# Kernel optimization log

Hardware: AMD Instinct MI355X
Metric: run time of the kernel (lower is better)

Reference implementation:

```python
import jax, jax.numpy as jnp
import numpy as np

N_NODES = 100000
N_EDGES = 1600000
N_GRAPHS = 1024
HID = 128
FINAL = 128
SPATIAL = 3
NUM_LAYERS = 3
VOCAB = 100


def _linear_params(key, d_in, d_out):
    k1, k2 = jax.random.split(key)
    s = 1.0 / np.sqrt(d_in)
    W = jax.random.uniform(k1, (d_out, d_in), jnp.float32, -s, s)
    b = jax.random.uniform(k2, (d_out,), jnp.float32, -s, s)
    return W, b


def setup_inputs() -> dict:
    key = jax.random.key(0)
    ks = jax.random.split(key, 16)
    z = jax.random.randint(ks[0], (N_NODES,), 0, VOCAB)
    pos = jax.random.normal(ks[1], (N_NODES, SPATIAL), jnp.float32)
    edge_index = jax.random.randint(ks[2], (2, N_EDGES), 0, N_NODES)
    batch = jnp.sort(jax.random.randint(ks[3], (N_NODES,), 0, N_GRAPHS))
    emb_table = jax.random.normal(ks[4], (VOCAB, HID), jnp.float32)
    W_pos, b_pos = _linear_params(ks[5], SPATIAL, HID)
    W_comb, b_comb = _linear_params(ks[6], 2 * HID, HID)
    # GIN: each conv's MLP is Linear(d,d) -> ReLU -> Linear(d,d); all dims 128 here.
    gW1, gb1, gW2, gb2 = [], [], [], []
    for i in range(NUM_LAYERS):
        k = jax.random.fold_in(ks[7], i)
        ka, kb = jax.random.split(k)
        W1, b1 = _linear_params(ka, HID, HID)
        W2, b2 = _linear_params(kb, HID, FINAL if i == NUM_LAYERS - 1 else HID)
        gW1.append(W1); gb1.append(b1); gW2.append(W2); gb2.append(b2)
    gin_W1 = jnp.stack(gW1); gin_b1 = jnp.stack(gb1)
    gin_W2 = jnp.stack(gW2); gin_b2 = jnp.stack(gb2)
    W_p1, b_p1 = _linear_params(ks[8], FINAL, FINAL)
    W_p2, b_p2 = _linear_params(ks[9], FINAL, 1)
    return {
        "z": z, "pos": pos, "edge_index": edge_index, "batch": batch,
        "emb_table": emb_table, "W_pos": W_pos, "b_pos": b_pos,
        "W_comb": W_comb, "b_comb": b_comb,
        "gin_W1": gin_W1, "gin_b1": gin_b1, "gin_W2": gin_W2, "gin_b2": gin_b2,
        "W_p1": W_p1, "b_p1": b_p1, "W_p2": W_p2, "b_p2": b_p2,
    }


def reference(z, pos, edge_index, batch, emb_table, W_pos, b_pos, W_comb, b_comb,
              gin_W1, gin_b1, gin_W2, gin_b2, W_p1, b_p1, W_p2, b_p2):
    src, dst = edge_index[0], edge_index[1]
    # initial node embedding: embed(z) || linear(pos) -> linear -> relu
    atom = emb_table[z]                                   # [N, H]
    pe = pos @ W_pos.T + b_pos                            # [N, H]
    x = jax.nn.relu(jnp.concatenate([atom, pe], axis=-1) @ W_comb.T + b_comb)
    # GIN layers: x' = MLP((1+eps)*x + sum_{j->i} x_j), eps=0; act between convs only
    for i in range(NUM_LAYERS):
        aggr = jax.ops.segment_sum(x[src], dst, num_segments=N_NODES)  # [N, H]
        h = aggr + x
        h = jax.nn.relu(h @ gin_W1[i].T + gin_b1[i])
        x = h @ gin_W2[i].T + gin_b2[i]
        if i < NUM_LAYERS - 1:
            x = jax.nn.relu(x)
    # sum pooling per graph, then predict MLP
    g = jax.ops.segment_sum(x, batch, num_segments=N_GRAPHS)  # [G, F]
    h = jax.nn.relu(g @ W_p1.T + b_p1)
    return h @ W_p2.T + b_p2                              # [G, 1]
```

## Files before the change

kernel.cpp:

```cpp
#include <hip/hip_runtime.h>
#include <hip/hip_bf16.h>

#define HID 128
#define CAP 64
#define NBK 2048

typedef __attribute__((ext_vector_type(8))) short bfrag;
typedef __attribute__((ext_vector_type(4))) float f32x4;

static inline size_t align256(size_t x) { return (x + 255) & ~(size_t)255; }

__device__ __forceinline__ unsigned short f2bf(float f) {
  unsigned int x = __float_as_uint(f);
  unsigned int r = x + 0x7fffu + ((x >> 16) & 1u);
  return (unsigned short)(r >> 16);
}
__device__ __forceinline__ float bflo(unsigned int u) { return __uint_as_float(u << 16); }
__device__ __forceinline__ float bfhi(unsigned int u) { return __uint_as_float(u & 0xffff0000u); }


__global__ __launch_bounds__(256) void k_prep(const int* __restrict__ src,
                                              const int* __restrict__ dst,
                                              int* __restrict__ cnt,
                                              int* __restrict__ bsrc, int E, int N,
                                              const float* __restrict__ W_comb,
                                              const float* __restrict__ gW1,
                                              const float* __restrict__ gW2,
                                              unsigned short* __restrict__ Wcb,
                                              unsigned short* __restrict__ W1b,
                                              unsigned short* __restrict__ W2b,
                                              const int* __restrict__ batch,
                                              int* __restrict__ goff, int G) {
  const int bid = blockIdx.x;
  const int tid = threadIdx.x;
  if (bid < NBK) {
    const int slice = bid & 7;
    const int sidx = bid >> 3;
    const int s_lo = (int)(((long long)slice * N) >> 3);
    const int s_hi = (int)(((long long)(slice + 1) * N) >> 3);
    for (int e = sidx * 256 + tid; e < E; e += (NBK / 8) * 256) {
      int d = dst[e];
      if (d >= s_lo && d < s_hi) {
        int slot = atomicAdd(&cnt[d], 1);
        if (slot < CAP) bsrc[(size_t)d * CAP + slot] = src[e];
      }
    }
  } else if (bid < NBK + 192) {
    int i = (bid - NBK) * 256 + tid;
    if (i < 128 * 256) Wcb[i] = f2bf(W_comb[i]);
    if (i < 3 * 128 * 128) {
      W1b[i] = f2bf(gW1[i]);
      W2b[i] = f2bf(gW2[i]);
    }
  } else {
    int g = (bid - NBK - 192) * 256 + tid;
    if (g <= G) {
      int lo = 0, hi = N;
      while (lo < hi) {
        int mid = (lo + hi) >> 1;
        if (batch[mid] < g) lo = mid + 1; else hi = mid;
      }
      goff[g] = lo;
    }
  }
}


__global__ __launch_bounds__(256, 2) void k_init_mm(const int* __restrict__ z,
                                                    const float* __restrict__ pos,
                                                    const float* __restrict__ emb,
                                                    const float* __restrict__ W_pos,
                                                    const float* __restrict__ b_pos,
                                                    const unsigned short* __restrict__ Wcb,
                                                    const float* __restrict__ bias,
                                                    const unsigned short* __restrict__ W1n,
                                                    unsigned short* __restrict__ Y, int n) {
  __shared__ unsigned int sE[32 * 128];
  __shared__ unsigned int sB[32 * 64];
  const int t = threadIdx.x;
  const int w = t >> 6, l = t & 63, lr = l & 15, lk = l >> 4;

  bfrag wcf[2][8];
#pragma unroll
  for (int s = 0; s < 2; ++s)
#pragma unroll
    for (int ks = 0; ks < 8; ++ks)
      wcf[s][ks] = *(const bfrag*)(Wcb + (size_t)(32 * w + 16 * s + lr) * 256 + ks * 32 + lk * 8);
  bfrag w1f[2][4];
#pragma unroll
  for (int s = 0; s < 2; ++s)
#pragma unroll
    for (int ks = 0; ks < 4; ++ks)
      w1f[s][ks] = *(const bfrag*)(W1n + (size_t)(32 * w + 16 * s + lr) * HID + ks * 32 + lk * 8);
  const float bias0 = bias[32 * w + lr];
  const float bias1 = bias[32 * w + 16 + lr];

  const int m0 = blockIdx.x * 32;
  {
    const int r = t >> 3, i = t & 7;
    int node = m0 + r;
    if (node >= n) node = n - 1;
    const int zz = z[node];
    const float p0 = pos[node * 3 + 0], p1 = pos[node * 3 + 1], p2 = pos[node * 3 + 2];
    const int swz = (r & 7) << 2;
#pragma unroll
    for (int k = 0; k < 16; ++k) {
      const int j = i + k * 8;
      float v0, v1;
      if (j < 64) {
        const float2 ev = *(const float2*)&emb[(size_t)zz * 128 + 2 * j];
        v0 = ev.x; v1 = ev.y;
      } else {
        const int f0 = 2 * j - 128;
        v0 = b_pos[f0] + W_pos[f0 * 3] * p0 + W_pos[f0 * 3 + 1] * p1 + W_pos[f0 * 3 + 2] * p2;
        v1 = b_pos[f0 + 1] + W_pos[f0 * 3 + 3] * p0 + W_pos[f0 * 3 + 4] * p1 +
             W_pos[f0 * 3 + 5] * p2;
      }
      sE[r * 128 + (j ^ swz)] = (unsigned int)f2bf(v0) | ((unsigned int)f2bf(v1) << 16);
    }
  }
  __syncthreads();

  f32x4 acc00 = {0.f, 0.f, 0.f, 0.f}, acc01 = acc00, acc10 = acc00, acc11 = acc00;
#pragma unroll
  for (int mt = 0; mt < 2; ++mt) {
    const int row = 16 * mt + lr;
    const int swz = (row & 7) << 2;
#pragma unroll
    for (int ks = 0; ks < 8; ++ks) {
      const bfrag a = *(const bfrag*)&sE[row * 128 + ((ks * 16 + lk * 4) ^ swz)];
      if (mt == 0) {
        acc00 = __builtin_amdgcn_mfma_f32_16x16x32_bf16(a, wcf[0][ks], acc00, 0, 0, 0);
        acc01 = __builtin_amdgcn_mfma_f32_16x16x32_bf16(a, wcf[1][ks], acc01, 0, 0, 0);
      } else {
        acc10 = __builtin_amdgcn_mfma_f32_16x16x32_bf16(a, wcf[0][ks], acc10, 0, 0, 0);
        acc11 = __builtin_amdgcn_mfma_f32_16x16x32_bf16(a, wcf[1][ks], acc11, 0, 0, 0);
      }
    }
  }
  {
    unsigned short* sB16 = (unsigned short*)sB;
#pragma unroll
    for (int mt = 0; mt < 2; ++mt) {
#pragma unroll
      for (int s = 0; s < 2; ++s) {
        const f32x4 a = mt == 0 ? (s == 0 ? acc00 : acc01) : (s == 0 ? acc10 : acc11);
        const float bb = s == 0 ? bias0 : bias1;
        const int col = 32 * w + 16 * s + lr;
#pragma unroll
        for (int r = 0; r < 4; ++r) {
          const int rowL = 16 * mt + 4 * lk + r;
          const int cu = (col >> 1) ^ ((rowL & 7) << 2);
          sB16[rowL * 128 + cu * 2 + (col & 1)] = f2bf(fmaxf(a[r] + bb, 0.f));
        }
      }
    }
  }
  __syncthreads();

  f32x4 u00 = {0.f, 0.f, 0.f, 0.f}, u01 = u00, u10 = u00, u11 = u00;
#pragma unroll
  for (int mt = 0; mt < 2; ++mt) {
    const int row = 16 * mt + lr;
    const int swz = (row & 7) << 2;
#pragma unroll
    for (int ks = 0; ks < 4; ++ks) {
      const bfrag a = *(const bfrag*)&sB[row * 64 + ((ks * 16 + lk * 4) ^ swz)];
      if (mt == 0) {
        u00 = __builtin_amdgcn_mfma_f32_16x16x32_bf16(a, w1f[0][ks], u00, 0, 0, 0);
        u01 = __builtin_amdgcn_mfma_f32_16x16x32_bf16(a, w1f[1][ks], u01, 0, 0, 0);
      } else {
        u10 = __builtin_amdgcn_mfma_f32_16x16x32_bf16(a, w1f[0][ks], u10, 0, 0, 0);
        u11 = __builtin_amdgcn_mfma_f32_16x16x32_bf16(a, w1f[1][ks], u11, 0, 0, 0);
      }
    }
  }
#pragma unroll
  for (int mt = 0; mt < 2; ++mt) {
#pragma unroll
    for (int s = 0; s < 2; ++s) {
      const f32x4 a = mt == 0 ? (s == 0 ? u00 : u01) : (s == 0 ? u10 : u11);
      const int col = 32 * w + 16 * s + lr;
#pragma unroll
      for (int r = 0; r < 4; ++r) {
        const int row = m0 + 16 * mt + 4 * lk + r;
        if (row < n) Y[(size_t)row * HID + col] = f2bf(a[r]);
      }
    }
  }
}


template <int LAST>
__global__ __launch_bounds__(256, 3) void k_layer(const unsigned int* __restrict__ U,
                                                  const int* __restrict__ cnt,
                                                  const int* __restrict__ bsrc,
                                                  const float* __restrict__ b1,
                                                  const unsigned short* __restrict__ W2b,
                                                  const float* __restrict__ b2,
                                                  const unsigned short* __restrict__ W1n,
                                                  unsigned short* __restrict__ Y, int n) {
  __shared__ unsigned int sA[32 * 64];
  __shared__ unsigned int sB[32 * 64];
  const int t = threadIdx.x;
  const int w = t >> 6, l = t & 63, lr = l & 15, lk = l >> 4;
  const int lgrp = lk, lpos = lr;

  bfrag w2f[2][4];
#pragma unroll
  for (int s = 0; s < 2; ++s)
#pragma unroll
    for (int ks = 0; ks < 4; ++ks)
      w2f[s][ks] = *(const bfrag*)(W2b + (size_t)(32 * w + 16 * s + lr) * HID + ks * 32 + lk * 8);
  bfrag w1f[2][4];
  if (!LAST) {
#pragma unroll
    for (int s = 0; s < 2; ++s)
#pragma unroll
      for (int ks = 0; ks < 4; ++ks)
        w1f[s][ks] = *(const bfrag*)(W1n + (size_t)(32 * w + 16 * s + lr) * HID + ks * 32 + lk * 8);
  }
  const float b2a = b2[32 * w + lr];
  const float b2b = b2[32 * w + 16 + lr];
  const float4 bb0 = *(const float4*)&b1[8 * lpos];
  const float4 bb1 = *(const float4*)&b1[8 * lpos + 4];
  const float ms = (lgrp == 0) ? 1.f : 0.f;

  const int m0 = blockIdx.x * 32;

  int degs[8];
  int eidxs[8];
#pragma unroll
  for (int ri = 0; ri < 8; ++ri) {
    int node = m0 + 8 * w + ri;
    if (node >= n) node = n - 1;
    int d = cnt[node];
    degs[ri] = d > CAP ? CAP : d;
    eidxs[ri] = bsrc[(size_t)node * CAP + l];
  }
#pragma unroll
  for (int ri = 0; ri < 8; ++ri) {
    const int row = 8 * w + ri;
    int node = m0 + row;
    if (node >= n) node = n - 1;
    const int deg = degs[ri];
    const int eidx = eidxs[ri];
    const uint4 sv = *(const uint4*)(U + (size_t)node * 64 + 4 * lpos);
    float a0 = ms * bflo(sv.x), a1 = ms * bfhi(sv.x);
    float a2 = ms * bflo(sv.y), a3 = ms * bfhi(sv.y);
    float a4 = ms * bflo(sv.z), a5 = ms * bfhi(sv.z);
    float a6 = ms * bflo(sv.w), a7 = ms * bfhi(sv.w);
    int k = 0;
    for (; k + 7 < deg; k += 8) {
      const int e0 = __shfl(eidx, k + lgrp);
      const int e1 = __shfl(eidx, k + 4 + lgrp);
      const uint4 u0 = *(const uint4*)(U + (size_t)e0 * 64 + 4 * lpos);
      const uint4 u1 = *(const uint4*)(U + (size_t)e1 * 64 + 4 * lpos);
      a0 += bflo(u0.x); a1 += bfhi(u0.x); a2 += bflo(u0.y); a3 += bfhi(u0.y);
      a4 += bflo(u0.z); a5 += bfhi(u0.z); a6 += bflo(u0.w); a7 += bfhi(u0.w);
      a0 += bflo(u1.x); a1 += bfhi(u1.x); a2 += bflo(u1.y); a3 += bfhi(u1.y);
      a4 += bflo(u1.z); a5 += bfhi(u1.z); a6 += bflo(u1.w); a7 += bfhi(u1.w);
    }
    for (; k < deg; k += 4) {
      int idx = k + lgrp;
      const float m = idx < deg ? 1.f : 0.f;
      if (idx >= deg) idx = deg - 1;
      const int e0 = __shfl(eidx, idx);
      const uint4 u0 = *(const uint4*)(U + (size_t)e0 * 64 + 4 * lpos);
      a0 += m * bflo(u0.x); a1 += m * bfhi(u0.x); a2 += m * bflo(u0.y); a3 += m * bfhi(u0.y);
      a4 += m * bflo(u0.z); a5 += m * bfhi(u0.z); a6 += m * bflo(u0.w); a7 += m * bfhi(u0.w);
    }
    a0 += __shfl_xor(a0, 16); a0 += __shfl_xor(a0, 32);
    a1 += __shfl_xor(a1, 16); a1 += __shfl_xor(a1, 32);
    a2 += __shfl_xor(a2, 16); a2 += __shfl_xor(a2, 32);
    a3 += __shfl_xor(a3, 16); a3 += __shfl_xor(a3, 32);
    a4 += __shfl_xor(a4, 16); a4 += __shfl_xor(a4, 32);
    a5 += __shfl_xor(a5, 16); a5 += __shfl_xor(a5, 32);
    a6 += __shfl_xor(a6, 16); a6 += __shfl_xor(a6, 32);
    a7 += __shfl_xor(a7, 16); a7 += __shfl_xor(a7, 32);
    if (lgrp == 0) {
      const int swz = (row & 7) << 2;
      uint4 o;
      o.x = (unsigned int)f2bf(fmaxf(a0 + bb0.x, 0.f)) |
            ((unsigned int)f2bf(fmaxf(a1 + bb0.y, 0.f)) << 16);
      o.y = (unsigned int)f2bf(fmaxf(a2 + bb0.z, 0.f)) |
            ((unsigned int)f2bf(fmaxf(a3 + bb0.w, 0.f)) << 16);
      o.z = (unsigned int)f2bf(fmaxf(a4 + bb1.x, 0.f)) |
            ((unsigned int)f2bf(fmaxf(a5 + bb1.y, 0.f)) << 16);
      o.w = (unsigned int)f2bf(fmaxf(a6 + bb1.z, 0.f)) |
            ((unsigned int)f2bf(fmaxf(a7 + bb1.w, 0.f)) << 16);
      *(uint4*)&sA[row * 64 + ((4 * lpos) ^ swz)] = o;
    }
  }
  __syncthreads();

  f32x4 acc00 = {0.f, 0.f, 0.f, 0.f}, acc01 = acc00, acc10 = acc00, acc11 = acc00;
#pragma unroll
  for (int mt = 0; mt < 2; ++mt) {
    const int row = 16 * mt + lr;
    const int swz = (row & 7) << 2;
#pragma unroll
    for (int ks = 0; ks < 4; ++ks) {
      const bfrag a = *(const bfrag*)&sA[row * 64 + ((ks * 16 + lk * 4) ^ swz)];
      if (mt == 0) {
        acc00 = __builtin_amdgcn_mfma_f32_16x16x32_bf16(a, w2f[0][ks], acc00, 0, 0, 0);
        acc01 = __builtin_amdgcn_mfma_f32_16x16x32_bf16(a, w2f[1][ks], acc01, 0, 0, 0);
      } else {
        acc10 = __builtin_amdgcn_mfma_f32_16x16x32_bf16(a, w2f[0][ks], acc10, 0, 0, 0);
        acc11 = __builtin_amdgcn_mfma_f32_16x16x32_bf16(a, w2f[1][ks], acc11, 0, 0, 0);
      }
    }
  }
  if (LAST) {
#pragma unroll
    for (int mt = 0; mt < 2; ++mt) {
#pragma unroll
      for (int s = 0; s < 2; ++s) {
        const f32x4 a = mt == 0 ? (s == 0 ? acc00 : acc01) : (s == 0 ? acc10 : acc11);
        const float bb = s == 0 ? b2a : b2b;
        const int col = 32 * w + 16 * s + lr;
#pragma unroll
        for (int r = 0; r < 4; ++r) {
          const int row = m0 + 16 * mt + 4 * lk + r;
          if (row < n) Y[(size_t)row * HID + col] = f2bf(a[r] + bb);
        }
      }
    }
  } else {
    unsigned short* sB16 = (unsigned short*)sB;
#pragma unroll
    for (int mt = 0; mt < 2; ++mt) {
#pragma unroll
      for (int s = 0; s < 2; ++s) {
        const f32x4 a = mt == 0 ? (s == 0 ? acc00 : acc01) : (s == 0 ? acc10 : acc11);
        const float bb = s == 0 ? b2a : b2b;
        const int col = 32 * w + 16 * s + lr;
#pragma unroll
        for (int r = 0; r < 4; ++r) {
          const int rowL = 16 * mt + 4 * lk + r;
          const int cu = (col >> 1) ^ ((rowL & 7) << 2);
          sB16[rowL * 128 + cu * 2 + (col & 1)] = f2bf(fmaxf(a[r] + bb, 0.f));
        }
      }
    }
    __syncthreads();
    f32x4 u00 = {0.f, 0.f, 0.f, 0.f}, u01 = u00, u10 = u00, u11 = u00;
#pragma unroll
    for (int mt = 0; mt < 2; ++mt) {
      const int row = 16 * mt + lr;
      const int swz = (row & 7) << 2;
#pragma unroll
      for (int ks = 0; ks < 4; ++ks) {
        const bfrag a = *(const bfrag*)&sB[row * 64 + ((ks * 16 + lk * 4) ^ swz)];
        if (mt == 0) {
          u00 = __builtin_amdgcn_mfma_f32_16x16x32_bf16(a, w1f[0][ks], u00, 0, 0, 0);
          u01 = __builtin_amdgcn_mfma_f32_16x16x32_bf16(a, w1f[1][ks], u01, 0, 0, 0);
        } else {
          u10 = __builtin_amdgcn_mfma_f32_16x16x32_bf16(a, w1f[0][ks], u10, 0, 0, 0);
          u11 = __builtin_amdgcn_mfma_f32_16x16x32_bf16(a, w1f[1][ks], u11, 0, 0, 0);
        }
      }
    }
#pragma unroll
    for (int mt = 0; mt < 2; ++mt) {
#pragma unroll
      for (int s = 0; s < 2; ++s) {
        const f32x4 a = mt == 0 ? (s == 0 ? u00 : u01) : (s == 0 ? u10 : u11);
        const int col = 32 * w + 16 * s + lr;
#pragma unroll
        for (int r = 0; r < 4; ++r) {
          const int row = m0 + 16 * mt + 4 * lk + r;
          if (row < n) Y[(size_t)row * HID + col] = f2bf(a[r]);
        }
      }
    }
  }
}


__global__ __launch_bounds__(128) void k_pool(const unsigned short* __restrict__ X,
                                              const int* __restrict__ goff,
                                              const float* __restrict__ Wp1,
                                              const float* __restrict__ bp1,
                                              const float* __restrict__ Wp2,
                                              const float* __restrict__ bp2,
                                              float* __restrict__ out, int G) {
  __shared__ float sg[HID];
  __shared__ float sred[HID];
  int g = blockIdx.x;
  int f = threadIdx.x;
  int n0 = goff[g], n1 = goff[g + 1];
  float c0 = 0.f, c1 = 0.f, c2 = 0.f, c3 = 0.f;
  int nn = n0;
  for (; nn + 3 < n1; nn += 4) {
    c0 += __uint_as_float((unsigned int)X[(size_t)nn * HID + f] << 16);
    c1 += __uint_as_float((unsigned int)X[(size_t)(nn + 1) * HID + f] << 16);
    c2 += __uint_as_float((unsigned int)X[(size_t)(nn + 2) * HID + f] << 16);
    c3 += __uint_as_float((unsigned int)X[(size_t)(nn + 3) * HID + f] << 16);
  }
  for (; nn < n1; ++nn) c0 += __uint_as_float((unsigned int)X[(size_t)nn * HID + f] << 16);
  sg[f] = (c0 + c1) + (c2 + c3);
  __syncthreads();
  float a0 = 0.f, a1 = 0.f, a2 = 0.f, a3 = 0.f;
#pragma unroll
  for (int k4 = 0; k4 < 32; ++k4) {
    float4 wv = *(const float4*)&Wp1[f * HID + k4 * 4];
    float4 xv = *(const float4*)&sg[k4 * 4];
    a0 += wv.x * xv.x; a1 += wv.y * xv.y; a2 += wv.z * xv.z; a3 += wv.w * xv.w;
  }
  float h = fmaxf(bp1[f] + ((a0 + a1) + (a2 + a3)), 0.f);
  sred[f] = Wp2[f] * h;
  __syncthreads();
  for (int s = 64; s > 0; s >>= 1) {
    if (f < s) sred[f] += sred[f + s];
    __syncthreads();
  }
  if (f == 0) out[g] = sred[0] + bp2[0];
}


extern "C" void kernel_launch(void* const* d_in, const int* in_sizes, int n_in,
                              void* d_out, int out_size, void* d_ws, size_t ws_size,
                              hipStream_t stream) {
  const int*   z      = (const int*)d_in[0];
  const float* pos    = (const float*)d_in[1];
  const int*   ei     = (const int*)d_in[2];
  const int*   batch  = (const int*)d_in[3];
  const float* emb    = (const float*)d_in[4];
  const float* W_pos  = (const float*)d_in[5];
  const float* b_pos  = (const float*)d_in[6];
  const float* W_comb = (const float*)d_in[7];
  const float* b_comb = (const float*)d_in[8];
  const float* gW1    = (const float*)d_in[9];
  const float* gb1    = (const float*)d_in[10];
  const float* gW2    = (const float*)d_in[11];
  const float* gb2    = (const float*)d_in[12];
  const float* Wp1    = (const float*)d_in[13];
  const float* bp1    = (const float*)d_in[14];
  const float* Wp2    = (const float*)d_in[15];
  const float* bp2    = (const float*)d_in[16];
  float* out = (float*)d_out;

  const int N = in_sizes[0];
  const int E = in_sizes[2] / 2;
  const int G = out_size;
  const int* srcp = ei;
  const int* dstp = ei + E;
  const int ntiles = (N + 31) / 32;

  char* w = (char*)d_ws;
  unsigned short* Ub  = (unsigned short*)w; w += align256((size_t)N * 128 * 2);
  unsigned short* Vb  = (unsigned short*)w; w += align256((size_t)N * 128 * 2);
  unsigned short* Wcb = (unsigned short*)w; w += align256((size_t)128 * 256 * 2);
  unsigned short* W1b = (unsigned short*)w; w += align256((size_t)3 * 128 * 128 * 2);
  unsigned short* W2b = (unsigned short*)w; w += align256((size_t)3 * 128 * 128 * 2);
  int* cnt  = (int*)w; w += align256((size_t)N * 4);
  int* bsrc = (int*)w; w += align256((size_t)N * CAP * 4);
  int* goff = (int*)w; w += align256((size_t)(G + 1) * 4);

  hipMemsetAsync(cnt, 0, (size_t)N * 4, stream);

  k_prep<<<NBK + 192 + 5, 256, 0, stream>>>(srcp, dstp, cnt, bsrc, E, N,
                                            W_comb, gW1, gW2, Wcb, W1b, W2b,
                                            batch, goff, G);

  k_init_mm<<<ntiles, 256, 0, stream>>>(z, pos, emb, W_pos, b_pos, Wcb, b_comb,
                                        W1b, Ub, N);

  k_layer<0><<<ntiles, 256, 0, stream>>>((const unsigned int*)Ub, cnt, bsrc, gb1,
                                         W2b, gb2, W1b + (size_t)1 * 128 * 128, Vb, N);
  k_layer<0><<<ntiles, 256, 0, stream>>>((const unsigned int*)Vb, cnt, bsrc, gb1 + 128,
                                         W2b + (size_t)1 * 128 * 128, gb2 + 128,
                                         W1b + (size_t)2 * 128 * 128, Ub, N);
  k_layer<1><<<ntiles, 256, 0, stream>>>((const unsigned int*)Ub, cnt, bsrc, gb1 + 256,
                                         W2b + (size_t)2 * 128 * 128, gb2 + 256,
                                         (const unsigned short*)nullptr, Vb, N);

  k_pool<<<G, HID, 0, stream>>>(Vb, goff, Wp1, bp1, Wp2, bp2, out, G);
}
```

Before: 431.9 us.

## Merge prep and init kernels; pad gather with zero sentinel row

Fuses the CSR-bucket/weight-conversion prep kernel and the initial embedding matmul into one launch. The init blocks now convert W_comb and layer-0 W1 to bf16 straight from fp32 instead of waiting for a converted copy, which removes one launch and the dependency between them. The layer gather loop now rounds each degree up to a multiple of 8 and sends padded slots to an extra all-zero row N in U/V, so the masked tail loop goes away. The cost is some extra zero-row loads and the extra per-block conversion work in the init blocks.

```diff
diff --git a/kernel.cpp b/kernel.cpp
--- a/kernel.cpp
+++ b/kernel.cpp
@@ -4,6 +4,7 @@
 #define HID 128
 #define CAP 64
 #define NBK 2048
+#define NWC 192
 
 typedef __attribute__((ext_vector_type(8))) short bfrag;
 typedef __attribute__((ext_vector_type(4))) float f32x4;
@@ -18,21 +19,35 @@
 __device__ __forceinline__ float bflo(unsigned int u) { return __uint_as_float(u << 16); }
 __device__ __forceinline__ float bfhi(unsigned int u) { return __uint_as_float(u & 0xffff0000u); }
 
-
-__global__ __launch_bounds__(256) void k_prep(const int* __restrict__ src,
-                                              const int* __restrict__ dst,
-                                              int* __restrict__ cnt,
-                                              int* __restrict__ bsrc, int E, int N,
-                                              const float* __restrict__ W_comb,
-                                              const float* __restrict__ gW1,
-                                              const float* __restrict__ gW2,
-                                              unsigned short* __restrict__ Wcb,
-                                              unsigned short* __restrict__ W1b,
-                                              unsigned short* __restrict__ W2b,
-                                              const int* __restrict__ batch,
-                                              int* __restrict__ goff, int G) {
+__device__ __forceinline__ bfrag load8bf(const float* __restrict__ p) {
+  const float4 a = *(const float4*)p;
+  const float4 b = *(const float4*)(p + 4);
+  bfrag r;
+  r[0] = (short)f2bf(a.x); r[1] = (short)f2bf(a.y);
+  r[2] = (short)f2bf(a.z); r[3] = (short)f2bf(a.w);
+  r[4] = (short)f2bf(b.x); r[5] = (short)f2bf(b.y);
+  r[6] = (short)f2bf(b.z); r[7] = (short)f2bf(b.w);
+  return r;
+}
+
+
+__global__ __launch_bounds__(256, 2) void k_mega(
+    const int* __restrict__ src, const int* __restrict__ dst,
+    int* __restrict__ cnt, int* __restrict__ bsrc, int E, int N,
+    const float* __restrict__ gW1, const float* __restrict__ gW2,
+    unsigned short* __restrict__ W1b, unsigned short* __restrict__ W2b,
+    const int* __restrict__ batch, int* __restrict__ goff, int G, int initBase,
+    const int* __restrict__ z, const float* __restrict__ pos,
+    const float* __restrict__ emb, const float* __restrict__ W_pos,
+    const float* __restrict__ b_pos, const float* __restrict__ W_comb,
+    const float* __restrict__ b_comb,
+    unsigned int* __restrict__ UbZ, unsigned int* __restrict__ VbZ,
+    unsigned short* __restrict__ Y, int n) {
+  __shared__ unsigned int sE[32 * 128];
+  __shared__ unsigned int sB[32 * 64];
   const int bid = blockIdx.x;
   const int tid = threadIdx.x;
+
   if (bid < NBK) {
     const int slice = bid & 7;
     const int sidx = bid >> 3;
@@ -45,15 +60,18 @@
         if (slot < CAP) bsrc[(size_t)d * CAP + slot] = src[e];
       }
     }
-  } else if (bid < NBK + 192) {
+    return;
+  }
+  if (bid < NBK + NWC) {
     int i = (bid - NBK) * 256 + tid;
-    if (i < 128 * 256) Wcb[i] = f2bf(W_comb[i]);
     if (i < 3 * 128 * 128) {
       W1b[i] = f2bf(gW1[i]);
       W2b[i] = f2bf(gW2[i]);
     }
-  } else {
-    int g = (bid - NBK - 192) * 256 + tid;
+    return;
+  }
+  if (bid < initBase) {
+    int g = (bid - NBK - NWC) * 256 + tid;
     if (g <= G) {
       int lo = 0, hi = N;
       while (lo < hi) {
@@ -62,42 +80,33 @@
       }
       goff[g] = lo;
     }
-  }
-}
-
-
-__global__ __launch_bounds__(256, 2) void k_init_mm(const int* __restrict__ z,
-                                                    const float* __restrict__ pos,
-                                                    const float* __restrict__ emb,
-                                                    const float* __restrict__ W_pos,
-                                                    const float* __restrict__ b_pos,
-                                                    const unsigned short* __restrict__ Wcb,
-                                                    const float* __restrict__ bias,
-                                                    const unsigned short* __restrict__ W1n,
-                                                    unsigned short* __restrict__ Y, int n) {
-  __shared__ unsigned int sE[32 * 128];
-  __shared__ unsigned int sB[32 * 64];
-  const int t = threadIdx.x;
-  const int w = t >> 6, l = t & 63, lr = l & 15, lk = l >> 4;
+    if (bid == initBase - 1) {
+      if (tid >= 64 && tid < 128) UbZ[tid - 64] = 0;
+      else if (tid >= 128 && tid < 192) VbZ[tid - 128] = 0;
+    }
+    return;
+  }
+
+  const int w = tid >> 6, l = tid & 63, lr = l & 15, lk = l >> 4;
 
   bfrag wcf[2][8];
 #pragma unroll
   for (int s = 0; s < 2; ++s)
 #pragma unroll
     for (int ks = 0; ks < 8; ++ks)
-      wcf[s][ks] = *(const bfrag*)(Wcb + (size_t)(32 * w + 16 * s + lr) * 256 + ks * 32 + lk * 8);
+      wcf[s][ks] = load8bf(&W_comb[(size_t)(32 * w + 16 * s + lr) * 256 + ks * 32 + lk * 8]);
   bfrag w1f[2][4];
 #pragma unroll
   for (int s = 0; s < 2; ++s)
 #pragma unroll
     for (int ks = 0; ks < 4; ++ks)
-      w1f[s][ks] = *(const bfrag*)(W1n + (size_t)(32 * w + 16 * s + lr) * HID + ks * 32 + lk * 8);
-  const float bias0 = bias[32 * w + lr];
-  const float bias1 = bias[32 * w + 16 + lr];
-
-  const int m0 = blockIdx.x * 32;
+      w1f[s][ks] = load8bf(&gW1[(size_t)(32 * w + 16 * s + lr) * HID + ks * 32 + lk * 8]);
+  const float bias0 = b_comb[32 * w + lr];
+  const float bias1 = b_comb[32 * w + 16 + lr];
+
+  const int m0 = (bid - initBase) * 32;
   {
-    const int r = t >> 3, i = t & 7;
+    const int r = tid >> 3, i = tid & 7;
     int node = m0 + r;
     if (node >= n) node = n - 1;
     const int zz = z[node];
@@ -235,23 +244,24 @@
     int node = m0 + 8 * w + ri;
     if (node >= n) node = n - 1;
     int d = cnt[node];
-    degs[ri] = d > CAP ? CAP : d;
-    eidxs[ri] = bsrc[(size_t)node * CAP + l];
+    d = d > CAP ? CAP : d;
+    degs[ri] = d;
+    const int e = bsrc[(size_t)node * CAP + l];
+    eidxs[ri] = (l < d) ? e : n;
   }
 #pragma unroll
   for (int ri = 0; ri < 8; ++ri) {
     const int row = 8 * w + ri;
     int node = m0 + row;
     if (node >= n) node = n - 1;
-    const int deg = degs[ri];
+    const int deg8 = (degs[ri] + 7) & ~7;
     const int eidx = eidxs[ri];
     const uint4 sv = *(const uint4*)(U + (size_t)node * 64 + 4 * lpos);
     float a0 = ms * bflo(sv.x), a1 = ms * bfhi(sv.x);
     float a2 = ms * bflo(sv.y), a3 = ms * bfhi(sv.y);
     float a4 = ms * bflo(sv.z), a5 = ms * bfhi(sv.z);
     float a6 = ms * bflo(sv.w), a7 = ms * bfhi(sv.w);
-    int k = 0;
-    for (; k + 7 < deg; k += 8) {
+    for (int k = 0; k < deg8; k += 8) {
       const int e0 = __shfl(eidx, k + lgrp);
       const int e1 = __shfl(eidx, k + 4 + lgrp);
       const uint4 u0 = *(const uint4*)(U + (size_t)e0 * 64 + 4 * lpos);
@@ -260,15 +270,6 @@
       a4 += bflo(u0.z); a5 += bfhi(u0.z); a6 += bflo(u0.w); a7 += bfhi(u0.w);
       a0 += bflo(u1.x); a1 += bfhi(u1.x); a2 += bflo(u1.y); a3 += bfhi(u1.y);
       a4 += bflo(u1.z); a5 += bfhi(u1.z); a6 += bflo(u1.w); a7 += bfhi(u1.w);
-    }
-    for (; k < deg; k += 4) {
-      int idx = k + lgrp;
-      const float m = idx < deg ? 1.f : 0.f;
-      if (idx >= deg) idx = deg - 1;
-      const int e0 = __shfl(eidx, idx);
-      const uint4 u0 = *(const uint4*)(U + (size_t)e0 * 64 + 4 * lpos);
-      a0 += m * bflo(u0.x); a1 += m * bfhi(u0.x); a2 += m * bflo(u0.y); a3 += m * bfhi(u0.y);
-      a4 += m * bflo(u0.z); a5 += m * bfhi(u0.z); a6 += m * bflo(u0.w); a7 += m * bfhi(u0.w);
     }
     a0 += __shfl_xor(a0, 16); a0 += __shfl_xor(a0, 32);
     a1 += __shfl_xor(a1, 16); a1 += __shfl_xor(a1, 32);
@@ -447,11 +448,12 @@
   const int* srcp = ei;
   const int* dstp = ei + E;
   const int ntiles = (N + 31) / 32;
+  const int nGoff = (G + 1 + 255) / 256;
+  const int initBase = NBK + NWC + nGoff;
 
   char* w = (char*)d_ws;
-  unsigned short* Ub  = (unsigned short*)w; w += align256((size_t)N * 128 * 2);
-  unsigned short* Vb  = (unsigned short*)w; w += align256((size_t)N * 128 * 2);
-  unsigned short* Wcb = (unsigned short*)w; w += align256((size_t)128 * 256 * 2);
+  unsigned short* Ub  = (unsigned short*)w; w += align256((size_t)(N + 1) * 128 * 2);
+  unsigned short* Vb  = (unsigned short*)w; w += align256((size_t)(N + 1) * 128 * 2);
   unsigned short* W1b = (unsigned short*)w; w += align256((size_t)3 * 128 * 128 * 2);
   unsigned short* W2b = (unsigned short*)w; w += align256((size_t)3 * 128 * 128 * 2);
   int* cnt  = (int*)w; w += align256((size_t)N * 4);
@@ -460,12 +462,10 @@
 
   hipMemsetAsync(cnt, 0, (size_t)N * 4, stream);
 
-  k_prep<<<NBK + 192 + 5, 256, 0, stream>>>(srcp, dstp, cnt, bsrc, E, N,
-                                            W_comb, gW1, gW2, Wcb, W1b, W2b,
-                                            batch, goff, G);
-
-  k_init_mm<<<ntiles, 256, 0, stream>>>(z, pos, emb, W_pos, b_pos, Wcb, b_comb,
-                                        W1b, Ub, N);
+  k_mega<<<initBase + ntiles, 256, 0, stream>>>(
+      srcp, dstp, cnt, bsrc, E, N, gW1, gW2, W1b, W2b, batch, goff, G, initBase,
+      z, pos, emb, W_pos, b_pos, W_comb, b_comb,
+      (unsigned int*)(Ub + (size_t)N * 128), (unsigned int*)(Vb + (size_t)N * 128), Ub, N);
 
   k_layer<0><<<ntiles, 256, 0, stream>>>((const unsigned int*)Ub, cnt, bsrc, gb1,
                                          W2b, gb2, W1b + (size_t)1 * 128 * 128, Vb, N);
```

Measured after the change: 483.9 us. 1.12x slower.
